# Kernel optimization log

Measured on AMD Instinct MI355X. Metric: run time of the kernel, lower is better.

## Reference

```python
import jax, jax.numpy as jnp
import numpy as np

D_MODEL = 256
D_FFN = 1024
N_LEVELS = 4
N_HEADS = 8
N_POINTS = 4
HEAD_DIM = D_MODEL // N_HEADS
SPATIAL = [(128, 128), (64, 64), (32, 32), (16, 16)]
LQ = sum(h * w for h, w in SPATIAL)  # 21760
B = 2


def setup_inputs() -> dict:
    key = jax.random.key(0)
    ks = jax.random.split(key, 24)

    def w(k, shape, s=0.02):
        return (jax.random.normal(k, shape) * s).astype(jnp.float32)

    HLP = N_HEADS * N_LEVELS * N_POINTS
    starts = np.cumsum([0] + [h * w_ for h, w_ in SPATIAL[:-1]])
    return {
        "src": jax.random.normal(ks[0], (B, LQ, D_MODEL), jnp.float32),
        "pos": 0.1 * jax.random.normal(ks[1], (B, LQ, D_MODEL), jnp.float32),
        "reference_points": jax.random.uniform(ks[2], (B, LQ, N_LEVELS, 2), jnp.float32),
        "W_off": w(ks[3], (D_MODEL, HLP * 2)),
        "b_off": w(ks[4], (HLP * 2,), 0.5),
        "W_attn": w(ks[5], (D_MODEL, HLP)),
        "b_attn": jnp.zeros((HLP,), jnp.float32),
        "W_val": w(ks[6], (D_MODEL, D_MODEL)),
        "b_val": jnp.zeros((D_MODEL,), jnp.float32),
        "W_out": w(ks[7], (D_MODEL, D_MODEL)),
        "b_out": jnp.zeros((D_MODEL,), jnp.float32),
        "ln1_g": jnp.ones((D_MODEL,), jnp.float32),
        "ln1_b": jnp.zeros((D_MODEL,), jnp.float32),
        "W1": w(ks[8], (D_MODEL, D_FFN)),
        "b1": jnp.zeros((D_FFN,), jnp.float32),
        "W2": w(ks[9], (D_FFN, D_MODEL)),
        "b2": jnp.zeros((D_MODEL,), jnp.float32),
        "ln2_g": jnp.ones((D_MODEL,), jnp.float32),
        "ln2_b": jnp.zeros((D_MODEL,), jnp.float32),
        "spatial_shapes": np.array(SPATIAL, np.int32),
        "level_start_index": np.array(starts, np.int32),
    }


def _layernorm(x, g, b):
    mu = x.mean(-1, keepdims=True)
    var = ((x - mu) ** 2).mean(-1, keepdims=True)
    return (x - mu) * jax.lax.rsqrt(var + 1e-5) * g + b


def _bilinear_sample(v, x, y, H, W):
    # v: [N, H, W, D]; x, y: [N, Lq, P] pixel coords (align_corners=False, zero pad)
    x0f = jnp.floor(x)
    y0f = jnp.floor(y)
    x0 = x0f.astype(jnp.int32)
    y0 = y0f.astype(jnp.int32)
    wx1 = x - x0f
    wy1 = y - y0f
    wx0 = 1.0 - wx1
    wy0 = 1.0 - wy1
    vf = v.reshape(v.shape[0], H * W, v.shape[-1])

    def gather(xi, yi, wt):
        valid = (xi >= 0) & (xi < W) & (yi >= 0) & (yi < H)
        idx = jnp.clip(yi, 0, H - 1) * W + jnp.clip(xi, 0, W - 1)
        g = jnp.take_along_axis(vf, idx.reshape(idx.shape[0], -1)[..., None], axis=1)
        g = g.reshape(*xi.shape, vf.shape[-1])
        return g * (wt * valid.astype(wt.dtype))[..., None]

    return (gather(x0, y0, wx0 * wy0) + gather(x0 + 1, y0, wx1 * wy0)
            + gather(x0, y0 + 1, wx0 * wy1) + gather(x0 + 1, y0 + 1, wx1 * wy1))


def _ms_deform_attn(query, src, reference_points, W_off, b_off, W_attn, b_attn,
                    W_val, b_val, W_out, b_out, spatial_shapes):
    Bq, Lq, _ = query.shape
    ss = np.asarray(spatial_shapes)
    value = (src @ W_val + b_val).reshape(Bq, Lq, N_HEADS, HEAD_DIM)
    off = (query @ W_off + b_off).reshape(Bq, Lq, N_HEADS, N_LEVELS, N_POINTS, 2)
    attn = (query @ W_attn + b_attn).reshape(Bq, Lq, N_HEADS, N_LEVELS * N_POINTS)
    attn = jax.nn.softmax(attn, axis=-1).reshape(Bq, Lq, N_HEADS, N_LEVELS, N_POINTS)
    # offset normalizer = (W, H) per level
    normalizer = jnp.asarray(ss[:, ::-1].astype(np.float32))  # [L, 2]
    loc = reference_points[:, :, None, :, None, :] + off / normalizer[None, None, None, :, None, :]
    # loc: [B, Lq, M, L, P, 2] normalized in [0,1]
    out = jnp.zeros((Bq, N_HEADS, Lq, HEAD_DIM), query.dtype)
    start = 0
    for lvl in range(N_LEVELS):
        H, W = int(ss[lvl, 0]), int(ss[lvl, 1])
        v = value[:, start:start + H * W]                                 # [B, HW, M, D]
        v = v.transpose(0, 2, 1, 3).reshape(Bq * N_HEADS, H, W, HEAD_DIM)
        l = loc[:, :, :, lvl]                                             # [B, Lq, M, P, 2]
        x = (l[..., 0] * W - 0.5).transpose(0, 2, 1, 3).reshape(Bq * N_HEADS, Lq, N_POINTS)
        y = (l[..., 1] * H - 0.5).transpose(0, 2, 1, 3).reshape(Bq * N_HEADS, Lq, N_POINTS)
        sampled = _bilinear_sample(v, x, y, H, W)                         # [BM, Lq, P, D]
        wgt = attn[:, :, :, lvl].transpose(0, 2, 1, 3).reshape(Bq * N_HEADS, Lq, N_POINTS)
        out = out + (sampled * wgt[..., None]).sum(2).reshape(Bq, N_HEADS, Lq, HEAD_DIM)
        start += H * W
    out = out.transpose(0, 2, 1, 3).reshape(Bq, Lq, D_MODEL)
    return out @ W_out + b_out


def reference(src, pos, reference_points, W_off, b_off, W_attn, b_attn, W_val, b_val,
              W_out, b_out, ln1_g, ln1_b, W1, b1, W2, b2, ln2_g, ln2_b,
              spatial_shapes, level_start_index):
    query = src + pos
    src2 = _ms_deform_attn(query, src, reference_points, W_off, b_off, W_attn, b_attn,
                           W_val, b_val, W_out, b_out, spatial_shapes)
    h = _layernorm(src + src2, ln1_g, ln1_b)
    ffn = jax.nn.relu(h @ W1 + b1) @ W2 + b2
    return _layernorm(h + ffn, ln2_g, ln2_b)
```

## Files before the change

### kernel.cpp

```cpp
#include <hip/hip_runtime.h>

typedef __bf16 bf16x8 __attribute__((ext_vector_type(8)));
typedef float f32x4 __attribute__((ext_vector_type(4)));

static constexpr int TOKS = 43520;
static constexpr int LQN  = 21760;

__device__ __forceinline__ unsigned short f2bf(float f) {
  union { float f; unsigned u; } v; v.f = f;
  return (unsigned short)((v.u + 0x7fffu + ((v.u >> 16) & 1u)) >> 16);
}
__device__ __forceinline__ float bf2f(unsigned short b) {
  union { unsigned u; float f; } v; v.u = ((unsigned)b) << 16; return v.f;
}

__global__ __launch_bounds__(256) void prewt_kernel(
    const float* __restrict__ src, const float* __restrict__ pos,
    unsigned short* __restrict__ srcb, unsigned short* __restrict__ qb,
    const float* __restrict__ W_val, const float* __restrict__ W_off,
    const float* __restrict__ W_attn, const float* __restrict__ W_out,
    const float* __restrict__ W1, const float* __restrict__ W2,
    const float* __restrict__ b_off, const float* __restrict__ b_attn,
    unsigned short* __restrict__ Wt_val, unsigned short* __restrict__ Wt_oa,
    unsigned short* __restrict__ Wt_out,
    unsigned short* __restrict__ Wt_1, unsigned short* __restrict__ Wt_2,
    float* __restrict__ b_oa) {
  const int bid = blockIdx.x;
  if (bid < 10880) {
    int i = bid * 256 + threadIdx.x;
    float4 s = ((const float4*)src)[i], p = ((const float4*)pos)[i];
    ((ushort4*)srcb)[i] = make_ushort4(f2bf(s.x), f2bf(s.y), f2bf(s.z), f2bf(s.w));
    ((ushort4*)qb)[i]   = make_ushort4(f2bf(s.x + p.x), f2bf(s.y + p.y),
                                       f2bf(s.z + p.z), f2bf(s.w + p.w));
    return;
  }
  int gid = (bid - 10880) * 256 + threadIdx.x;
  if (gid >= 754048) return;
  if (gid >= 753664) {
    int i = gid - 753664;
    b_oa[i] = (i < 256) ? b_off[i] : b_attn[i - 256];
    return;
  }
  const float* W; unsigned short* Wt; int idx, K, nsh;
  if (gid < 65536)       { W = W_val;  Wt = Wt_val;          idx = gid;          K = 256;  nsh = 8;  }
  else if (gid < 131072) { W = W_off;  Wt = Wt_oa;           idx = gid - 65536;  K = 256;  nsh = 8;  }
  else if (gid < 163840) { W = W_attn; Wt = Wt_oa + 65536;   idx = gid - 131072; K = 256;  nsh = 7;  }
  else if (gid < 229376) { W = W_out;  Wt = Wt_out;          idx = gid - 163840; K = 256;  nsh = 8;  }
  else if (gid < 491520) { W = W1;     Wt = Wt_1;            idx = gid - 229376; K = 256;  nsh = 10; }
  else                   { W = W2;     Wt = Wt_2;            idx = gid - 491520; K = 1024; nsh = 8;  }
  int k = idx >> nsh, n = idx & ((1 << nsh) - 1);
  Wt[n * K + k] = f2bf(W[idx]);
}

template <int K, int OUTOP>
__device__ __forceinline__ void gemm_body(unsigned short* __restrict__ As,
                                          unsigned short* __restrict__ Bs,
                                          const unsigned short* __restrict__ A,
                                          const unsigned short* __restrict__ Bt,
                                          const float* __restrict__ bias,
                                          const unsigned short* __restrict__ res,
                                          unsigned short* __restrict__ Cp,
                                          int N, int bm, int bn) {
  const int t = threadIdx.x;
  const int wave = t >> 6, lane = t & 63;
  const int wm = (wave & 1) << 6, wn = (wave >> 1) << 6;
  const int lr = lane & 15, lq = lane >> 4;
  const int row0 = t >> 2, cb0 = (t & 3) << 3;
  f32x4 acc[4][4] = {};
  const unsigned short* ga = A  + (size_t)(bm * 128 + row0) * K + cb0;
  const unsigned short* gb = Bt + (size_t)(bn * 128 + row0) * K + cb0;
  const size_t gs = (size_t)64 * K;
  uint4 pa0 = *(const uint4*)ga;
  uint4 pa1 = *(const uint4*)(ga + gs);
  uint4 pb0 = *(const uint4*)gb;
  uint4 pb1 = *(const uint4*)(gb + gs);
#pragma unroll 1
  for (int k0 = 0; k0 < K; k0 += 32) {
    __syncthreads();
    *(uint4*)&As[row0 * 40 + cb0] = pa0;
    *(uint4*)&As[(row0 + 64) * 40 + cb0] = pa1;
    *(uint4*)&Bs[row0 * 40 + cb0] = pb0;
    *(uint4*)&Bs[(row0 + 64) * 40 + cb0] = pb1;
    __syncthreads();
    if (k0 + 32 < K) {
      pa0 = *(const uint4*)(ga + k0 + 32);
      pa1 = *(const uint4*)(ga + gs + k0 + 32);
      pb0 = *(const uint4*)(gb + k0 + 32);
      pb1 = *(const uint4*)(gb + gs + k0 + 32);
    }
    bf16x8 af[4], bfr[4];
#pragma unroll
    for (int i = 0; i < 4; i++) af[i] = *(const bf16x8*)&As[(wm + i * 16 + lr) * 40 + lq * 8];
#pragma unroll
    for (int j = 0; j < 4; j++) bfr[j] = *(const bf16x8*)&Bs[(wn + j * 16 + lr) * 40 + lq * 8];
#pragma unroll
    for (int i = 0; i < 4; i++)
#pragma unroll
      for (int j = 0; j < 4; j++)
        acc[i][j] = __builtin_amdgcn_mfma_f32_16x16x32_bf16(af[i], bfr[j], acc[i][j], 0, 0, 0);
  }
  const int rb = bm * 128 + wm + lq * 4;
  const int cbase = bn * 128 + wn + lr;
#pragma unroll
  for (int j = 0; j < 4; j++) {
    const int col = cbase + j * 16;
    const float bv = bias[col];
#pragma unroll
    for (int i = 0; i < 4; i++) {
#pragma unroll
      for (int r = 0; r < 4; r++) {
        float v = acc[i][j][r] + bv;
        size_t o = (size_t)(rb + i * 16 + r) * N + col;
        if (OUTOP == 1) Cp[o] = f2bf(v);
        else if (OUTOP == 2) Cp[o] = f2bf(fmaxf(v, 0.f));
        else Cp[o] = f2bf(v + bf2f(res[o]));
      }
    }
  }
}

__global__ __launch_bounds__(256) void proj_kernel(
    const unsigned short* __restrict__ srcb, const unsigned short* __restrict__ qb,
    const unsigned short* __restrict__ Wt_val, const unsigned short* __restrict__ Wt_oa,
    const float* __restrict__ b_val, const float* __restrict__ b_oa,
    unsigned short* __restrict__ valb, unsigned short* __restrict__ oab) {
  __shared__ unsigned short As[128 * 40];
  __shared__ unsigned short Bs[128 * 40];
  const int bn = blockIdx.y;
  if (bn < 2)
    gemm_body<256, 1>(As, Bs, srcb, Wt_val, b_val, nullptr, valb, 256, blockIdx.x, bn);
  else
    gemm_body<256, 1>(As, Bs, qb, Wt_oa, b_oa, nullptr, oab, 384, blockIdx.x, bn - 2);
}

__global__ __launch_bounds__(256) void gemm_out_kernel(
    const unsigned short* __restrict__ A, const unsigned short* __restrict__ Bt,
    const float* __restrict__ bias, const unsigned short* __restrict__ res,
    unsigned short* __restrict__ C) {
  __shared__ unsigned short As[128 * 40];
  __shared__ unsigned short Bs[128 * 40];
  gemm_body<256, 3>(As, Bs, A, Bt, bias, res, C, 256, blockIdx.x, blockIdx.y);
}

__global__ __launch_bounds__(256) void gemm_ffn1_kernel(
    const unsigned short* __restrict__ A, const unsigned short* __restrict__ Bt,
    const float* __restrict__ bias, unsigned short* __restrict__ C) {
  __shared__ unsigned short As[128 * 40];
  __shared__ unsigned short Bs[128 * 40];
  gemm_body<256, 2>(As, Bs, A, Bt, bias, nullptr, C, 1024, blockIdx.x, blockIdx.y);
}

__global__ __launch_bounds__(256) void gemm_ffn2_kernel(
    const unsigned short* __restrict__ A, const unsigned short* __restrict__ Bt,
    const float* __restrict__ bias, const unsigned short* __restrict__ res,
    unsigned short* __restrict__ C) {
  __shared__ unsigned short As[128 * 40];
  __shared__ unsigned short Bs[128 * 40];
  gemm_body<1024, 3>(As, Bs, A, Bt, bias, res, C, 256, blockIdx.x, blockIdx.y);
}

__device__ __forceinline__ void fma8(uint4 v, float w, float* a) {
  const unsigned uu[4] = {v.x, v.y, v.z, v.w};
#pragma unroll
  for (int i = 0; i < 4; i++) {
    union { unsigned u; float f; } lo, hi;
    lo.u = uu[i] << 16;
    hi.u = uu[i] & 0xffff0000u;
    a[2 * i]     += w * lo.f;
    a[2 * i + 1] += w * hi.f;
  }
}

__global__ __launch_bounds__(256) void deform_kernel(const unsigned short* __restrict__ valb,
                                                     const unsigned short* __restrict__ oab,
                                                     const float* __restrict__ refp,
                                                     unsigned short* __restrict__ outb) {
  __shared__ float4  sW[8][8][17];
  __shared__ ushort4 sI[8][8][17];
  const int t = threadIdx.x;
  const int bid = blockIdx.x;
  const int nb = (bid & 7) * 680 + (bid >> 3);
  const int tok0 = nb * 8;
  const int SD[4] = {128, 64, 32, 16};

  if (t < 64) {
    const int g = t >> 3, h = t & 7;
    const int tok = tok0 + g;
    const unsigned short* lg = oab + (size_t)tok * 384 + 256 + h * 16;
    uint4 lv0 = ((const uint4*)lg)[0];
    uint4 lv1 = ((const uint4*)lg)[1];
    const unsigned lw[8] = {lv0.x, lv0.y, lv0.z, lv0.w, lv1.x, lv1.y, lv1.z, lv1.w};
    float w[16];
#pragma unroll
    for (int i = 0; i < 8; i++) {
      union { unsigned u; float f; } lo, hi;
      lo.u = lw[i] << 16; hi.u = lw[i] & 0xffff0000u;
      w[2 * i] = lo.f; w[2 * i + 1] = hi.f;
    }
    float mx = -1e30f;
#pragma unroll
    for (int i = 0; i < 16; i++) mx = fmaxf(mx, w[i]);
    float s = 0.f;
#pragma unroll
    for (int i = 0; i < 16; i++) { w[i] = __expf(w[i] - mx); s += w[i]; }
    const float inv = 1.f / s;
    const unsigned short* of = oab + (size_t)tok * 384 + h * 32;
    uint4 o0 = ((const uint4*)of)[0], o1 = ((const uint4*)of)[1];
    uint4 o2 = ((const uint4*)of)[2], o3 = ((const uint4*)of)[3];
    const unsigned ow[16] = {o0.x, o0.y, o0.z, o0.w, o1.x, o1.y, o1.z, o1.w,
                             o2.x, o2.y, o2.z, o2.w, o3.x, o3.y, o3.z, o3.w};
    float off[32];
#pragma unroll
    for (int i = 0; i < 16; i++) {
      union { unsigned u; float f; } lo, hi;
      lo.u = ow[i] << 16; hi.u = ow[i] & 0xffff0000u;
      off[2 * i] = lo.f; off[2 * i + 1] = hi.f;
    }
    const float* rp = refp + (size_t)tok * 8;
#pragma unroll
    for (int l = 0; l < 4; l++) {
      const int S = SD[l];
      const float Sf = (float)S;
      const float rx = rp[l * 2 + 0] * Sf - 0.5f;
      const float ry = rp[l * 2 + 1] * Sf - 0.5f;
#pragma unroll
      for (int p = 0; p < 4; p++) {
        const int idx = l * 4 + p;
        const float x = rx + off[l * 8 + p * 2 + 0];
        const float y = ry + off[l * 8 + p * 2 + 1];
        const float aw = w[idx] * inv;
        const float x0f = floorf(x), y0f = floorf(y);
        const int x0 = (int)x0f, y0 = (int)y0f;
        const float fx = x - x0f, fy = y - y0f;
        const bool xin0 = (x0 >= 0) & (x0 < S), xin1 = (x0 + 1 >= 0) & (x0 + 1 < S);
        const bool yin0 = (y0 >= 0) & (y0 < S), yin1 = (y0 + 1 >= 0) & (y0 + 1 < S);
        const int xc0 = min(max(x0, 0), S - 1), xc1 = min(max(x0 + 1, 0), S - 1);
        const int yc0 = min(max(y0, 0), S - 1), yc1 = min(max(y0 + 1, 0), S - 1);
        sW[g][h][idx] = make_float4(aw * (1.f - fx) * (1.f - fy) * (float)(xin0 & yin0),
                                    aw * fx * (1.f - fy)         * (float)(xin1 & yin0),
                                    aw * (1.f - fx) * fy         * (float)(xin0 & yin1),
                                    aw * fx * fy                 * (float)(xin1 & yin1));
        sI[g][h][idx] = make_ushort4((unsigned short)(yc0 * S + xc0),
                                     (unsigned short)(yc0 * S + xc1),
                                     (unsigned short)(yc1 * S + xc0),
                                     (unsigned short)(yc1 * S + xc1));
      }
    }
  }
  __syncthreads();

  const int g = t >> 5, h = (t >> 2) & 7, dc = t & 3;
  const int tok = tok0 + g;
  const int b = tok / LQN;
  float acc[8] = {0.f, 0.f, 0.f, 0.f, 0.f, 0.f, 0.f, 0.f};
  const int ST[4] = {0, 16384, 20480, 21504};
#pragma unroll
  for (int l = 0; l < 4; l++) {
    const unsigned short* vb = valb + ((size_t)(b * LQN + ST[l])) * 256 + h * 32 + dc * 8;
#pragma unroll
    for (int p = 0; p < 4; p++) {
      float4  W4 = sW[g][h][l * 4 + p];
      ushort4 I4 = sI[g][h][l * 4 + p];
      uint4 v00 = *(const uint4*)(vb + (size_t)I4.x * 256);
      uint4 v10 = *(const uint4*)(vb + (size_t)I4.y * 256);
      uint4 v01 = *(const uint4*)(vb + (size_t)I4.z * 256);
      uint4 v11 = *(const uint4*)(vb + (size_t)I4.w * 256);
      fma8(v00, W4.x, acc);
      fma8(v10, W4.y, acc);
      fma8(v01, W4.z, acc);
      fma8(v11, W4.w, acc);
    }
  }
  unsigned o[4];
#pragma unroll
  for (int i = 0; i < 4; i++)
    o[i] = (unsigned)f2bf(acc[2 * i]) | ((unsigned)f2bf(acc[2 * i + 1]) << 16);
  *(uint4*)(outb + (size_t)tok * 256 + h * 32 + dc * 8) = make_uint4(o[0], o[1], o[2], o[3]);
}

template <int OUT_F32>
__global__ __launch_bounds__(256) void ln_kernel(const ushort4* __restrict__ in,
                                                 const float* __restrict__ g,
                                                 const float* __restrict__ beta,
                                                 void* __restrict__ outp) {
  const int wv = blockIdx.x * 4 + (threadIdx.x >> 6);
  const int lane = threadIdx.x & 63;
  const size_t idx = (size_t)wv * 64 + lane;
  ushort4 u = in[idx];
  float x0 = bf2f(u.x), x1 = bf2f(u.y), x2 = bf2f(u.z), x3 = bf2f(u.w);
  float sum = x0 + x1 + x2 + x3;
#pragma unroll
  for (int o = 32; o >= 1; o >>= 1) sum += __shfl_xor(sum, o, 64);
  const float mu = sum * (1.f / 256.f);
  float d0 = x0 - mu, d1 = x1 - mu, d2 = x2 - mu, d3 = x3 - mu;
  float ss = d0 * d0 + d1 * d1 + d2 * d2 + d3 * d3;
#pragma unroll
  for (int o = 32; o >= 1; o >>= 1) ss += __shfl_xor(ss, o, 64);
  const float rs = rsqrtf(ss * (1.f / 256.f) + 1e-5f);
  float4 gg = ((const float4*)g)[lane], bb = ((const float4*)beta)[lane];
  float y0 = d0 * rs * gg.x + bb.x;
  float y1 = d1 * rs * gg.y + bb.y;
  float y2 = d2 * rs * gg.z + bb.z;
  float y3 = d3 * rs * gg.w + bb.w;
  if (OUT_F32) ((float4*)outp)[idx] = make_float4(y0, y1, y2, y3);
  else ((ushort4*)outp)[idx] = make_ushort4(f2bf(y0), f2bf(y1), f2bf(y2), f2bf(y3));
}

extern "C" void kernel_launch(void* const* d_in, const int* in_sizes, int n_in,
                              void* d_out, int out_size, void* d_ws, size_t ws_size,
                              hipStream_t stream) {
  (void)in_sizes; (void)n_in; (void)out_size; (void)ws_size;
  const float* src    = (const float*)d_in[0];
  const float* pos    = (const float*)d_in[1];
  const float* refp   = (const float*)d_in[2];
  const float* W_off  = (const float*)d_in[3];
  const float* b_off  = (const float*)d_in[4];
  const float* W_attn = (const float*)d_in[5];
  const float* b_attn = (const float*)d_in[6];
  const float* W_val  = (const float*)d_in[7];
  const float* b_val  = (const float*)d_in[8];
  const float* W_out  = (const float*)d_in[9];
  const float* b_out  = (const float*)d_in[10];
  const float* ln1_g  = (const float*)d_in[11];
  const float* ln1_b  = (const float*)d_in[12];
  const float* W1     = (const float*)d_in[13];
  const float* b1     = (const float*)d_in[14];
  const float* W2     = (const float*)d_in[15];
  const float* b2     = (const float*)d_in[16];
  const float* ln2_g  = (const float*)d_in[17];
  const float* ln2_b  = (const float*)d_in[18];

  char* ws = (char*)d_ws;
  unsigned short* Wt_val = (unsigned short*)ws;
  unsigned short* Wt_oa  = Wt_val + 65536;
  unsigned short* Wt_out = Wt_oa + 98304;
  unsigned short* Wt_1   = Wt_out + 65536;
  unsigned short* Wt_2   = Wt_1 + 262144;
  float*          b_oa   = (float*)(Wt_2 + 262144);
  const size_t WPOOL = 2u * 1024 * 1024;

  const size_t SZ_bf = (size_t)TOKS * 256 * 2;
  const size_t SZ_oa = (size_t)TOKS * 384 * 2;

  unsigned short* srcb = (unsigned short*)(ws + WPOOL);
  unsigned short* qb   = (unsigned short*)(ws + WPOOL + SZ_bf);
  unsigned short* valb = (unsigned short*)(ws + WPOOL + 2 * SZ_bf);
  unsigned short* oab  = (unsigned short*)(ws + WPOOL + 3 * SZ_bf);
  unsigned short* h_bf = (unsigned short*)(ws + WPOOL + 3 * SZ_bf + SZ_oa);
  unsigned short* hb   = (unsigned short*)(ws + WPOOL + 3 * SZ_bf + SZ_oa + SZ_bf);
  unsigned short* attnoutb = qb;
  unsigned short* preLN1b  = valb;
  unsigned short* preLN2b  = valb;

  prewt_kernel<<<13826, 256, 0, stream>>>(src, pos, srcb, qb,
                                          W_val, W_off, W_attn, W_out, W1, W2, b_off, b_attn,
                                          Wt_val, Wt_oa, Wt_out, Wt_1, Wt_2, b_oa);

  proj_kernel<<<dim3(340, 5), 256, 0, stream>>>(srcb, qb, Wt_val, Wt_oa, b_val, b_oa,
                                                valb, oab);

  deform_kernel<<<TOKS / 8, 256, 0, stream>>>(valb, oab, refp, attnoutb);

  gemm_out_kernel<<<dim3(340, 2), 256, 0, stream>>>(attnoutb, Wt_out, b_out, srcb, preLN1b);
  ln_kernel<0><<<10880, 256, 0, stream>>>((const ushort4*)preLN1b, ln1_g, ln1_b, h_bf);

  gemm_ffn1_kernel<<<dim3(340, 8), 256, 0, stream>>>(h_bf, Wt_1, b1, hb);
  gemm_ffn2_kernel<<<dim3(340, 2), 256, 0, stream>>>(hb, Wt_2, b2, h_bf, preLN2b);

  ln_kernel<1><<<10880, 256, 0, stream>>>((const ushort4*)preLN2b, ln2_g, ln2_b, d_out);
}
```

Measured before the change: 441.8 us.

## Double-buffer GEMM LDS tiles and parallelize deform sampling setup across all threads

The shared GEMM body now alternates between two LDS buffers, which removes the leading barrier each K-step. The deform kernel spreads sampling-location and weight computation over all 256 threads, one per (token, head, level), instead of 64 threads each looping over four levels. It also stores byte offsets as int4 so the gather needs no per-load multiply. In exchange, LDS use per GEMM block doubles, which may lower occupancy, and each thread now recomputes the softmax redundantly.

```diff
diff --git a/kernel.cpp b/kernel.cpp
--- a/kernel.cpp
+++ b/kernel.cpp
@@ -74,13 +74,15 @@
   uint4 pa1 = *(const uint4*)(ga + gs);
   uint4 pb0 = *(const uint4*)gb;
   uint4 pb1 = *(const uint4*)(gb + gs);
+  int p = 0;
 #pragma unroll 1
   for (int k0 = 0; k0 < K; k0 += 32) {
-    __syncthreads();
-    *(uint4*)&As[row0 * 40 + cb0] = pa0;
-    *(uint4*)&As[(row0 + 64) * 40 + cb0] = pa1;
-    *(uint4*)&Bs[row0 * 40 + cb0] = pb0;
-    *(uint4*)&Bs[(row0 + 64) * 40 + cb0] = pb1;
+    unsigned short* Ab = As + p * 5120;
+    unsigned short* Bb = Bs + p * 5120;
+    *(uint4*)&Ab[row0 * 40 + cb0] = pa0;
+    *(uint4*)&Ab[(row0 + 64) * 40 + cb0] = pa1;
+    *(uint4*)&Bb[row0 * 40 + cb0] = pb0;
+    *(uint4*)&Bb[(row0 + 64) * 40 + cb0] = pb1;
     __syncthreads();
     if (k0 + 32 < K) {
       pa0 = *(const uint4*)(ga + k0 + 32);
@@ -90,14 +92,15 @@
     }
     bf16x8 af[4], bfr[4];
 #pragma unroll
-    for (int i = 0; i < 4; i++) af[i] = *(const bf16x8*)&As[(wm + i * 16 + lr) * 40 + lq * 8];
-#pragma unroll
-    for (int j = 0; j < 4; j++) bfr[j] = *(const bf16x8*)&Bs[(wn + j * 16 + lr) * 40 + lq * 8];
+    for (int i = 0; i < 4; i++) af[i] = *(const bf16x8*)&Ab[(wm + i * 16 + lr) * 40 + lq * 8];
+#pragma unroll
+    for (int j = 0; j < 4; j++) bfr[j] = *(const bf16x8*)&Bb[(wn + j * 16 + lr) * 40 + lq * 8];
 #pragma unroll
     for (int i = 0; i < 4; i++)
 #pragma unroll
       for (int j = 0; j < 4; j++)
         acc[i][j] = __builtin_amdgcn_mfma_f32_16x16x32_bf16(af[i], bfr[j], acc[i][j], 0, 0, 0);
+    p ^= 1;
   }
   const int rb = bm * 128 + wm + lq * 4;
   const int cbase = bn * 128 + wn + lr;
@@ -124,8 +127,8 @@
     const unsigned short* __restrict__ Wt_val, const unsigned short* __restrict__ Wt_oa,
     const float* __restrict__ b_val, const float* __restrict__ b_oa,
     unsigned short* __restrict__ valb, unsigned short* __restrict__ oab) {
-  __shared__ unsigned short As[128 * 40];
-  __shared__ unsigned short Bs[128 * 40];
+  __shared__ unsigned short As[2 * 5120];
+  __shared__ unsigned short Bs[2 * 5120];
   const int bn = blockIdx.y;
   if (bn < 2)
     gemm_body<256, 1>(As, Bs, srcb, Wt_val, b_val, nullptr, valb, 256, blockIdx.x, bn);
@@ -137,16 +140,16 @@
     const unsigned short* __restrict__ A, const unsigned short* __restrict__ Bt,
     const float* __restrict__ bias, const unsigned short* __restrict__ res,
     unsigned short* __restrict__ C) {
-  __shared__ unsigned short As[128 * 40];
-  __shared__ unsigned short Bs[128 * 40];
+  __shared__ unsigned short As[2 * 5120];
+  __shared__ unsigned short Bs[2 * 5120];
   gemm_body<256, 3>(As, Bs, A, Bt, bias, res, C, 256, blockIdx.x, blockIdx.y);
 }
 
 __global__ __launch_bounds__(256) void gemm_ffn1_kernel(
     const unsigned short* __restrict__ A, const unsigned short* __restrict__ Bt,
     const float* __restrict__ bias, unsigned short* __restrict__ C) {
-  __shared__ unsigned short As[128 * 40];
-  __shared__ unsigned short Bs[128 * 40];
+  __shared__ unsigned short As[2 * 5120];
+  __shared__ unsigned short Bs[2 * 5120];
   gemm_body<256, 2>(As, Bs, A, Bt, bias, nullptr, C, 1024, blockIdx.x, blockIdx.y);
 }
 
@@ -154,8 +157,8 @@
     const unsigned short* __restrict__ A, const unsigned short* __restrict__ Bt,
     const float* __restrict__ bias, const unsigned short* __restrict__ res,
     unsigned short* __restrict__ C) {
-  __shared__ unsigned short As[128 * 40];
-  __shared__ unsigned short Bs[128 * 40];
+  __shared__ unsigned short As[2 * 5120];
+  __shared__ unsigned short Bs[2 * 5120];
   gemm_body<1024, 3>(As, Bs, A, Bt, bias, res, C, 256, blockIdx.x, blockIdx.y);
 }
 
@@ -175,16 +178,15 @@
                                                      const unsigned short* __restrict__ oab,
                                                      const float* __restrict__ refp,
                                                      unsigned short* __restrict__ outb) {
-  __shared__ float4  sW[8][8][17];
-  __shared__ ushort4 sI[8][8][17];
+  __shared__ float4 sW[8][8][17];
+  __shared__ int4   sI[8][8][17];
   const int t = threadIdx.x;
   const int bid = blockIdx.x;
   const int nb = (bid & 7) * 680 + (bid >> 3);
   const int tok0 = nb * 8;
-  const int SD[4] = {128, 64, 32, 16};
-
-  if (t < 64) {
-    const int g = t >> 3, h = t & 7;
+
+  {
+    const int g = t >> 5, h = (t >> 2) & 7, l = t & 3;
     const int tok = tok0 + g;
     const unsigned short* lg = oab + (size_t)tok * 384 + 256 + h * 16;
     uint4 lv0 = ((const uint4*)lg)[0];
@@ -204,47 +206,39 @@
 #pragma unroll
     for (int i = 0; i < 16; i++) { w[i] = __expf(w[i] - mx); s += w[i]; }
     const float inv = 1.f / s;
-    const unsigned short* of = oab + (size_t)tok * 384 + h * 32;
-    uint4 o0 = ((const uint4*)of)[0], o1 = ((const uint4*)of)[1];
-    uint4 o2 = ((const uint4*)of)[2], o3 = ((const uint4*)of)[3];
-    const unsigned ow[16] = {o0.x, o0.y, o0.z, o0.w, o1.x, o1.y, o1.z, o1.w,
-                             o2.x, o2.y, o2.z, o2.w, o3.x, o3.y, o3.z, o3.w};
-    float off[32];
-#pragma unroll
-    for (int i = 0; i < 16; i++) {
+    uint4 ov = *(const uint4*)(oab + (size_t)tok * 384 + h * 32 + l * 8);
+    const unsigned owv[4] = {ov.x, ov.y, ov.z, ov.w};
+    float off[8];
+#pragma unroll
+    for (int i = 0; i < 4; i++) {
       union { unsigned u; float f; } lo, hi;
-      lo.u = ow[i] << 16; hi.u = ow[i] & 0xffff0000u;
+      lo.u = owv[i] << 16; hi.u = owv[i] & 0xffff0000u;
       off[2 * i] = lo.f; off[2 * i + 1] = hi.f;
     }
-    const float* rp = refp + (size_t)tok * 8;
-#pragma unroll
-    for (int l = 0; l < 4; l++) {
-      const int S = SD[l];
-      const float Sf = (float)S;
-      const float rx = rp[l * 2 + 0] * Sf - 0.5f;
-      const float ry = rp[l * 2 + 1] * Sf - 0.5f;
-#pragma unroll
-      for (int p = 0; p < 4; p++) {
-        const int idx = l * 4 + p;
-        const float x = rx + off[l * 8 + p * 2 + 0];
-        const float y = ry + off[l * 8 + p * 2 + 1];
-        const float aw = w[idx] * inv;
-        const float x0f = floorf(x), y0f = floorf(y);
-        const int x0 = (int)x0f, y0 = (int)y0f;
-        const float fx = x - x0f, fy = y - y0f;
-        const bool xin0 = (x0 >= 0) & (x0 < S), xin1 = (x0 + 1 >= 0) & (x0 + 1 < S);
-        const bool yin0 = (y0 >= 0) & (y0 < S), yin1 = (y0 + 1 >= 0) & (y0 + 1 < S);
-        const int xc0 = min(max(x0, 0), S - 1), xc1 = min(max(x0 + 1, 0), S - 1);
-        const int yc0 = min(max(y0, 0), S - 1), yc1 = min(max(y0 + 1, 0), S - 1);
-        sW[g][h][idx] = make_float4(aw * (1.f - fx) * (1.f - fy) * (float)(xin0 & yin0),
-                                    aw * fx * (1.f - fy)         * (float)(xin1 & yin0),
-                                    aw * (1.f - fx) * fy         * (float)(xin0 & yin1),
-                                    aw * fx * fy                 * (float)(xin1 & yin1));
-        sI[g][h][idx] = make_ushort4((unsigned short)(yc0 * S + xc0),
-                                     (unsigned short)(yc0 * S + xc1),
-                                     (unsigned short)(yc1 * S + xc0),
-                                     (unsigned short)(yc1 * S + xc1));
-      }
+    const float* rp = refp + (size_t)tok * 8 + l * 2;
+    const int S = 128 >> l;
+    const float Sf = (float)S;
+    const float rx = rp[0] * Sf - 0.5f;
+    const float ry = rp[1] * Sf - 0.5f;
+#pragma unroll
+    for (int p = 0; p < 4; p++) {
+      const int idx = l * 4 + p;
+      const float x = rx + off[p * 2 + 0];
+      const float y = ry + off[p * 2 + 1];
+      const float aw = w[idx] * inv;
+      const float x0f = floorf(x), y0f = floorf(y);
+      const int x0 = (int)x0f, y0 = (int)y0f;
+      const float fx = x - x0f, fy = y - y0f;
+      const bool xin0 = (x0 >= 0) & (x0 < S), xin1 = (x0 + 1 >= 0) & (x0 + 1 < S);
+      const bool yin0 = (y0 >= 0) & (y0 < S), yin1 = (y0 + 1 >= 0) & (y0 + 1 < S);
+      const int xc0 = min(max(x0, 0), S - 1), xc1 = min(max(x0 + 1, 0), S - 1);
+      const int yc0 = min(max(y0, 0), S - 1), yc1 = min(max(y0 + 1, 0), S - 1);
+      sW[g][h][idx] = make_float4(aw * (1.f - fx) * (1.f - fy) * (float)(xin0 & yin0),
+                                  aw * fx * (1.f - fy)         * (float)(xin1 & yin0),
+                                  aw * (1.f - fx) * fy         * (float)(xin0 & yin1),
+                                  aw * fx * fy                 * (float)(xin1 & yin1));
+      sI[g][h][idx] = make_int4((yc0 * S + xc0) << 9, (yc0 * S + xc1) << 9,
+                                (yc1 * S + xc0) << 9, (yc1 * S + xc1) << 9);
     }
   }
   __syncthreads();
@@ -256,15 +250,15 @@
   const int ST[4] = {0, 16384, 20480, 21504};
 #pragma unroll
   for (int l = 0; l < 4; l++) {
-    const unsigned short* vb = valb + ((size_t)(b * LQN + ST[l])) * 256 + h * 32 + dc * 8;
+    const char* vbc = (const char*)(valb + ((size_t)(b * LQN + ST[l])) * 256 + h * 32 + dc * 8);
 #pragma unroll
     for (int p = 0; p < 4; p++) {
-      float4  W4 = sW[g][h][l * 4 + p];
-      ushort4 I4 = sI[g][h][l * 4 + p];
-      uint4 v00 = *(const uint4*)(vb + (size_t)I4.x * 256);
-      uint4 v10 = *(const uint4*)(vb + (size_t)I4.y * 256);
-      uint4 v01 = *(const uint4*)(vb + (size_t)I4.z * 256);
-      uint4 v11 = *(const uint4*)(vb + (size_t)I4.w * 256);
+      float4 W4 = sW[g][h][l * 4 + p];
+      int4   I4 = sI[g][h][l * 4 + p];
+      uint4 v00 = *(const uint4*)(vbc + I4.x);
+      uint4 v10 = *(const uint4*)(vbc + I4.y);
+      uint4 v01 = *(const uint4*)(vbc + I4.z);
+      uint4 v11 = *(const uint4*)(vbc + I4.w);
       fma8(v00, W4.x, acc);
       fma8(v10, W4.y, acc);
       fma8(v01, W4.z, acc);
```

New measurement: 436.8 us. Within noise of the previous version (-1.1%).
